# Performance work log

Hardware: AMD Instinct MI355X
Metric: run time of the kernel (lower is better)

The kernel has to match this reference:

```python
import jax, jax.numpy as jnp
import numpy as np

B, S, D, H = 2, 2048, 1024, 16
DH = D // H
EPS = 1e-5


def setup_inputs() -> dict:
    key = jax.random.key(0)
    ks = jax.random.split(key, 12)
    inp = {
        "Q_source": jax.random.normal(ks[0], (B, S, D), jnp.float32),
        "K_source": jax.random.normal(ks[1], (B, S, D), jnp.float32),
        "V_source": jax.random.normal(ks[2], (B, S, D), jnp.float32),
        "padding_mask": jnp.zeros((B, 1, 1, S), dtype=bool),  # no padded keys (avoids NaN rows)
        "future_mask": jnp.triu(jnp.ones((S, S), dtype=bool), k=1)[None, None],  # causal
    }
    sc = 1.0 / np.sqrt(D)
    names = ["WQ", "WK", "WV", "WO"]
    for i, n in enumerate(names):
        inp[n] = jax.random.normal(ks[3 + i], (D, D), jnp.float32) * sc
        inp["b" + n[1]] = jnp.zeros((D,), jnp.float32)
    inp["gamma"] = jnp.ones((D,), jnp.float32)
    inp["beta"] = jnp.zeros((D,), jnp.float32)
    return inp


def reference(Q_source, K_source, V_source, padding_mask, future_mask,
              WQ, bQ, WK, bK, WV, bV, WO, bO, gamma, beta):
    b = Q_source.shape[0]
    # torch Linear: x @ W.T + b ; reshape to [B, H, S, DH]
    def proj(x, W, bb):
        y = x @ W.T + bb
        return y.reshape(b, -1, H, DH).transpose(0, 2, 1, 3)

    Q = proj(Q_source, WQ, bQ)
    K = proj(K_source, WK, bK)
    V = proj(V_source, WV, bV)

    scores = jnp.einsum("bhqd,bhkd->bhqk", Q, K) / jnp.sqrt(jnp.float32(DH))
    neg_inf = jnp.float32(-jnp.inf)
    scores = jnp.where(padding_mask, neg_inf, scores)
    scores = jnp.where(future_mask, neg_inf, scores)
    attn = jax.nn.softmax(scores, axis=-1)

    ctx = jnp.einsum("bhqk,bhkd->bhqd", attn, V)
    ctx = ctx.transpose(0, 2, 1, 3).reshape(b, -1, D)
    out = ctx @ WO.T + bO

    x = Q_source + out
    mu = x.mean(-1, keepdims=True)
    var = x.var(-1, keepdims=True)
    return (x - mu) * jax.lax.rsqrt(var + EPS) * gamma + beta
```

## Files before the change

### kernel.cpp

```cpp
#include <hip/hip_runtime.h>

#define S_LEN 2048
#define DMODEL 1024
#define NH 16
#define DHD 64

typedef __attribute__((ext_vector_type(8))) short bh8;
typedef __attribute__((ext_vector_type(4))) float f32x4;
typedef __attribute__((ext_vector_type(2))) unsigned int u32x2;
typedef __attribute__((ext_vector_type(4))) unsigned int u32x4;
typedef unsigned short u16;
typedef unsigned int u32;

static __device__ __forceinline__ u16 f2bf(float f) {
    unsigned u = __builtin_bit_cast(unsigned, f);
    u += 0x7fffu + ((u >> 16) & 1u);
    return (u16)(u >> 16);
}

typedef const __attribute__((address_space(1))) void* gptr_t;
typedef __attribute__((address_space(3))) void* lptr_t;

static __device__ __forceinline__ void gll16(const void* g, void* l) {
    __builtin_amdgcn_global_load_lds((gptr_t)g, (lptr_t)l, 16, 0, 0);
}

__global__ __launch_bounds__(256) void cvt_all(const float* __restrict__ WQ, const float* __restrict__ WK,
                                               const float* __restrict__ WV, const float* __restrict__ WO,
                                               const float* __restrict__ S0, const float* __restrict__ S1,
                                               const float* __restrict__ S2,
                                               u16* __restrict__ wq, u16* __restrict__ wk,
                                               u16* __restrict__ wv, u16* __restrict__ wo,
                                               u16* __restrict__ q0, u16* __restrict__ k0,
                                               u16* __restrict__ v0) {
    int bid = blockIdx.x;
    const float* s;
    u16* o;
    size_t base;
    if (bid < 2048) {
        int wi = bid >> 9;
        s = wi == 0 ? WQ : (wi == 1 ? WK : (wi == 2 ? WV : WO));
        o = wi == 0 ? wq : (wi == 1 ? wk : (wi == 2 ? wv : wo));
        base = (size_t)(bid & 511) * 2048;
    } else {
        int r = bid - 2048;
        int si = r >> 11;
        s = si == 0 ? S0 : (si == 1 ? S1 : S2);
        o = si == 0 ? q0 : (si == 1 ? k0 : v0);
        base = (size_t)(r & 2047) * 2048;
    }
    size_t i = base + (size_t)threadIdx.x * 8;
    float4 a = *(const float4*)(s + i);
    float4 b = *(const float4*)(s + i + 4);
    u32 p0 = (u32)f2bf(a.x) | ((u32)f2bf(a.y) << 16);
    u32 p1 = (u32)f2bf(a.z) | ((u32)f2bf(a.w) << 16);
    u32 p2 = (u32)f2bf(b.x) | ((u32)f2bf(b.y) << 16);
    u32 p3 = (u32)f2bf(b.z) | ((u32)f2bf(b.w) << 16);
    *(u32x4*)(o + i) = (u32x4){p0, p1, p2, p3};
}

template <int BM, int OBF, int AF32>
static __device__ __forceinline__ void gemm_body(const void* __restrict__ Ap, const u16* __restrict__ Bm,
                                                 const float* __restrict__ bias, void* __restrict__ Cv,
                                                 int N, int K, int bi, int bj, short* Al, short* Bl,
                                                 float oscale) {
    constexpr int MI = BM / 32;
    constexpr int NC = BM / 64;
    int tid = threadIdx.x, lane = tid & 63, w = tid >> 6;
    int ln = lane & 15, hi = lane >> 4;
    int wm = w >> 1, wn = w & 1;
    f32x4 acc[MI][4];
#pragma unroll
    for (int i = 0; i < MI; i++)
#pragma unroll
        for (int j = 0; j < 4; j++) acc[i][j] = (f32x4){0.f, 0.f, 0.f, 0.f};
    int nk = K >> 5;

    float4 fa[NC][2];
    auto loadA = [&](int kt) {
#pragma unroll
        for (int c = 0; c < NC; ++c) {
            int o = c * 4096 + tid * 16;
            int row = o >> 6, e0 = (o & 63) >> 1;
            const float* src = (const float*)Ap + (size_t)(bi * BM + row) * K + kt * 32 + e0;
            fa[c][0] = *(const float4*)src;
            fa[c][1] = *(const float4*)(src + 4);
        }
    };
    auto writeA = [&](int buf) {
#pragma unroll
        for (int c = 0; c < NC; ++c) {
            int o = c * 4096 + tid * 16;
            u32 w0 = (u32)f2bf(fa[c][0].x) | ((u32)f2bf(fa[c][0].y) << 16);
            u32 w1 = (u32)f2bf(fa[c][0].z) | ((u32)f2bf(fa[c][0].w) << 16);
            u32 w2 = (u32)f2bf(fa[c][1].x) | ((u32)f2bf(fa[c][1].y) << 16);
            u32 w3 = (u32)f2bf(fa[c][1].z) | ((u32)f2bf(fa[c][1].w) << 16);
            *(u32x4*)((char*)(Al + buf * (BM * 32)) + o) = (u32x4){w0, w1, w2, w3};
        }
    };
    auto stageA_lds = [&](int buf, int kt) {
#pragma unroll
        for (int c = 0; c < NC; ++c) {
            int o = c * 4096 + tid * 16;
            int row = o >> 6, col = (o & 63) >> 1;
            gll16((const u16*)Ap + (size_t)(bi * BM + row) * K + kt * 32 + col,
                  (char*)(Al + buf * (BM * 32)) + o);
        }
    };
    auto stageB = [&](int buf, int kt) {
#pragma unroll
        for (int c = 0; c < 2; ++c) {
            int o = c * 4096 + tid * 16;
            int row = o >> 6, col = (o & 63) >> 1;
            gll16(Bm + (size_t)(bj * 128 + row) * K + kt * 32 + col, (char*)(Bl + buf * 4096) + o);
        }
    };

    if constexpr (AF32) { loadA(0); writeA(0); } else { stageA_lds(0, 0); }
    stageB(0, 0);
    __syncthreads();
    int cur = 0;
    for (int kt = 0; kt < nk; ++kt) {
        bool pre = (kt + 1 < nk);
        if (pre) {
            if constexpr (AF32) loadA(kt + 1); else stageA_lds(cur ^ 1, kt + 1);
            stageB(cur ^ 1, kt + 1);
        }
        bh8 av[MI], bv[4];
#pragma unroll
        for (int i = 0; i < MI; i++) av[i] = *(const bh8*)&Al[cur * (BM * 32) + (wm * (BM / 2) + i * 16 + ln) * 32 + hi * 8];
#pragma unroll
        for (int j = 0; j < 4; j++) bv[j] = *(const bh8*)&Bl[cur * 4096 + (wn * 64 + j * 16 + ln) * 32 + hi * 8];
#pragma unroll
        for (int i = 0; i < MI; i++)
#pragma unroll
            for (int j = 0; j < 4; j++)
                acc[i][j] = __builtin_amdgcn_mfma_f32_16x16x32_bf16(av[i], bv[j], acc[i][j], 0, 0, 0);
        if constexpr (AF32) { if (pre) writeA(cur ^ 1); }
        __syncthreads();
        cur ^= 1;
    }
    if constexpr (OBF == 2) {
#pragma unroll
        for (int j = 0; j < 4; j++) {
            int col = wn * 64 + j * 16 + ln;
            float bvs = bias[bj * 128 + col];
#pragma unroll
            for (int i = 0; i < MI; i++) {
                int row0 = wm * (BM / 2) + i * 16 + hi * 4;
                u32 p01 = (u32)f2bf(acc[i][j][0] + bvs) | ((u32)f2bf(acc[i][j][1] + bvs) << 16);
                u32 p23 = (u32)f2bf(acc[i][j][2] + bvs) | ((u32)f2bf(acc[i][j][3] + bvs) << 16);
                int idx = col * 128 + (row0 ^ ((col & 7) << 3));
                *(u32x2*)&Al[idx] = (u32x2){p01, p23};
            }
        }
        __syncthreads();
        int b = bi >> 4;
        int sbase = (bi & 15) * 128;
#pragma unroll
        for (int it = 0; it < 8; ++it) {
            int idx = it * 256 + tid;
            int dcol = idx >> 4;
            int sl = (idx & 15) * 8;
            bh8 v = *(const bh8*)&Al[dcol * 128 + (sl ^ ((dcol & 7) << 3))];
            int h = bj * 2 + (dcol >> 6), d = dcol & 63;
            *(bh8*)((u16*)Cv + ((size_t)((b * 16 + h) * 64 + d)) * 2048 + sbase + sl) = v;
        }
        return;
    }
#pragma unroll
    for (int j = 0; j < 4; j++) {
        int col = bj * 128 + wn * 64 + j * 16 + ln;
        float bvs = bias[col];
#pragma unroll
        for (int i = 0; i < MI; i++) {
            int row0 = bi * BM + wm * (BM / 2) + i * 16 + hi * 4;
#pragma unroll
            for (int rr = 0; rr < 4; rr++) {
                if (OBF) {
                    float v = (acc[i][j][rr] + bvs) * oscale;
                    ((u16*)Cv)[(size_t)(row0 + rr) * N + col] = f2bf(v);
                } else {
                    ((float*)Cv)[(size_t)(row0 + rr) * N + col] = acc[i][j][rr] + bvs;
                }
            }
        }
    }
}

__global__ __launch_bounds__(256, 3) void gemm_qkv(const u16* __restrict__ A0, const u16* __restrict__ A1,
                                                   const u16* __restrict__ A2, const u16* __restrict__ B0,
                                                   const u16* __restrict__ B1, const u16* __restrict__ B2,
                                                   const float* __restrict__ c0, const float* __restrict__ c1,
                                                   const float* __restrict__ c2, u16* __restrict__ C0,
                                                   u16* __restrict__ C1, u16* __restrict__ VT) {
    __shared__ short SH[16384];
    short* Al = SH;
    short* Bl = SH + 8192;
    int bid = blockIdx.x;
    int swz = (bid & 7) * 96 + (bid >> 3);
    int z = swz >> 8, t = swz & 255;
    if (z == 2) {
        gemm_body<128, 2, 0>(A2, B2, c2, VT, 1024, 1024, t >> 3, t & 7, Al, Bl, 1.0f);
    } else if (z == 0) {
        gemm_body<128, 1, 0>(A0, B0, c0, C0, 1024, 1024, t >> 3, t & 7, Al, Bl, 0.18033688f);
    } else {
        gemm_body<128, 1, 0>(A1, B1, c1, C1, 1024, 1024, t >> 3, t & 7, Al, Bl, 1.0f);
    }
}

__global__ __launch_bounds__(512, 4) void gemm_o(const u16* __restrict__ A, const u16* __restrict__ Bm,
                                                 const float* __restrict__ bias, float* __restrict__ C) {
    __shared__ short Al[2 * 64 * 32];
    __shared__ short Bl[2 * 128 * 32];
    int tid = threadIdx.x, lane = tid & 63, w = tid >> 6;
    int ln = lane & 15, hi = lane >> 4;
    int wm = w >> 2, wn = w & 3;
    int bid = blockIdx.x;
    int swz = (bid & 7) * 64 + (bid >> 3);
    int bi = swz >> 3, bj = swz & 7;
    f32x4 acc[2][2];
#pragma unroll
    for (int i = 0; i < 2; i++)
#pragma unroll
        for (int j = 0; j < 2; j++) acc[i][j] = (f32x4){0.f, 0.f, 0.f, 0.f};

    auto stageA = [&](int buf, int kt) {
        if (tid < 256) {
            int o = tid * 16;
            int row = o >> 6, col = (o & 63) >> 1;
            gll16(A + (size_t)(bi * 64 + row) * 1024 + kt * 32 + col, (char*)(Al + buf * 2048) + o);
        }
    };
    auto stageB = [&](int buf, int kt) {
        int o = tid * 16;
        int row = o >> 6, col = (o & 63) >> 1;
        gll16(Bm + (size_t)(bj * 128 + row) * 1024 + kt * 32 + col, (char*)(Bl + buf * 4096) + o);
    };

    stageA(0, 0);
    stageB(0, 0);
    __syncthreads();
    int cur = 0;
    for (int kt = 0; kt < 32; ++kt) {
        if (kt + 1 < 32) {
            stageA(cur ^ 1, kt + 1);
            stageB(cur ^ 1, kt + 1);
        }
        bh8 av[2], bv[2];
#pragma unroll
        for (int i = 0; i < 2; i++) av[i] = *(const bh8*)&Al[cur * 2048 + (wm * 32 + i * 16 + ln) * 32 + hi * 8];
#pragma unroll
        for (int j = 0; j < 2; j++) bv[j] = *(const bh8*)&Bl[cur * 4096 + (wn * 32 + j * 16 + ln) * 32 + hi * 8];
#pragma unroll
        for (int i = 0; i < 2; i++)
#pragma unroll
            for (int j = 0; j < 2; j++)
                acc[i][j] = __builtin_amdgcn_mfma_f32_16x16x32_bf16(av[i], bv[j], acc[i][j], 0, 0, 0);
        __syncthreads();
        cur ^= 1;
    }
#pragma unroll
    for (int j = 0; j < 2; j++) {
        int col = bj * 128 + wn * 32 + j * 16 + ln;
        float bvs = bias[col];
#pragma unroll
        for (int i = 0; i < 2; i++) {
            int row0 = bi * 64 + wm * 32 + i * 16 + hi * 4;
#pragma unroll
            for (int rr = 0; rr < 4; rr++)
                C[(size_t)(row0 + rr) * 1024 + col] = acc[i][j][rr] + bvs;
        }
    }
}

template <int PLO, int PHI>
static __device__ __forceinline__ void attn_core(const u16* __restrict__ Qp, const u16* __restrict__ Kp,
                                                 const u16* __restrict__ VT, u16* __restrict__ Ctx,
                                                 short* Klb, short* Vlb, short* Pw, float* Csh, float* Ls,
                                                 int b, int h, int bh, int qt, int tid) {
    int lane = tid & 63, w = tid >> 6;
    int grp = w >> 2;
    int qsub = w & 3;
    int tgl = tid & 255;
    int ln = lane & 15, hi = lane >> 4;
    __builtin_amdgcn_s_setprio(PLO);
    bh8 ones;
#pragma unroll
    for (int e = 0; e < 8; e++) ones[e] = (short)0x3F80;

    auto stage_kv = [&](int buf, int kt) {
#pragma unroll
        for (int c = 0; c < 2; ++c) {
            int o = c * 4096 + tgl * 16;
            int rr = o >> 7;
            int slot = (o >> 4) & 7;
            gll16(Kp + ((size_t)(b * S_LEN + kt * 64 + rr)) * DMODEL + h * DHD + ((slot ^ (rr & 7)) << 3),
                  (char*)(Klb + buf * 4096) + o);
            gll16(VT + ((size_t)(bh * DHD + rr)) * S_LEN + kt * 64 + ((slot ^ (rr & 7)) << 3),
                  (char*)(Vlb + buf * 4096) + o);
        }
    };

    int nh = qt + 1;
    int nt = 2 * qt + 2;
    int kbase = grp * nh;
    int qg0 = (qt << 7) + qsub * 32 + ln;
    const bh8* qr0 = (const bh8*)(Qp + ((size_t)(b * S_LEN + qg0)) * DMODEL + h * DHD);
    const bh8* qr1 = (const bh8*)(Qp + ((size_t)(b * S_LEN + qg0 + 16)) * DMODEL + h * DHD);
    bh8 qf[2][2];
    qf[0][0] = qr0[hi]; qf[0][1] = qr0[4 + hi];
    qf[1][0] = qr1[hi]; qf[1][1] = qr1[4 + hi];
    f32x4 ctxa[2][4];
    f32x4 lacc[2];
#pragma unroll
    for (int g = 0; g < 2; g++) {
        lacc[g] = (f32x4){0.f, 0.f, 0.f, 0.f};
#pragma unroll
        for (int i = 0; i < 4; i++) ctxa[g][i] = (f32x4){0.f, 0.f, 0.f, 0.f};
    }
    stage_kv(0, kbase);
    __syncthreads();
    int cur = 0;
    for (int i = 0; i < nh; ++i) {
        int kt = kbase + i;
        if (i + 1 < nh) stage_kv(cur ^ 1, kt + 1);
        f32x4 sc[2][4];
#pragma unroll
        for (int g = 0; g < 2; g++)
#pragma unroll
            for (int ks = 0; ks < 4; ++ks) sc[g][ks] = (f32x4){0.f, 0.f, 0.f, 0.f};
        __builtin_amdgcn_s_setprio(PHI);
#pragma unroll
        for (int dwin = 0; dwin < 2; ++dwin) {
#pragma unroll
            for (int ks = 0; ks < 4; ++ks) {
                int rr = ks * 16 + ln;
                bh8 kv = *(const bh8*)&Klb[cur * 4096 + rr * 64 + ((dwin * 32 + hi * 8) ^ ((rr & 7) << 3))];
                sc[0][ks] = __builtin_amdgcn_mfma_f32_16x16x32_bf16(kv, qf[0][dwin], sc[0][ks], 0, 0, 0);
                sc[1][ks] = __builtin_amdgcn_mfma_f32_16x16x32_bf16(kv, qf[1][dwin], sc[1][ks], 0, 0, 0);
            }
        }
        __builtin_amdgcn_s_setprio(PLO);
        if (kt >= nt - 2) {
#pragma unroll
            for (int g = 0; g < 2; g++) {
                int qgq = qg0 + g * 16;
#pragma unroll
                for (int ks = 0; ks < 4; ++ks)
#pragma unroll
                    for (int rr = 0; rr < 4; ++rr) {
                        int kg = kt * 64 + ks * 16 + hi * 4 + rr;
                        sc[g][ks][rr] = (kg <= qgq) ? sc[g][ks][rr] : -1e30f;
                    }
            }
        }
#pragma unroll
        for (int g = 0; g < 2; g++) {
#pragma unroll
            for (int ks = 0; ks < 4; ++ks) {
                u32 u0 = __builtin_bit_cast(u32, __builtin_amdgcn_exp2f(sc[g][ks][0]));
                u32 u1 = __builtin_bit_cast(u32, __builtin_amdgcn_exp2f(sc[g][ks][1]));
                u32 u2 = __builtin_bit_cast(u32, __builtin_amdgcn_exp2f(sc[g][ks][2]));
                u32 u3 = __builtin_bit_cast(u32, __builtin_amdgcn_exp2f(sc[g][ks][3]));
                u32 a01 = (u0 >> 16) | (u1 & 0xffff0000u);
                u32 a23 = (u2 >> 16) | (u3 & 0xffff0000u);
                int kloc = ks * 16 + hi * 4;
                *(u32x2*)&Pw[(g * 16 + ln) * 64 + (kloc ^ ((ln & 7) << 3))] = (u32x2){a01, a23};
            }
        }
        __builtin_amdgcn_s_setprio(PHI);
#pragma unroll
        for (int kw = 0; kw < 2; ++kw) {
            bh8 pf0 = *(const bh8*)&Pw[ln * 64 + ((kw * 32 + hi * 8) ^ ((ln & 7) << 3))];
            bh8 pf1 = *(const bh8*)&Pw[(16 + ln) * 64 + ((kw * 32 + hi * 8) ^ ((ln & 7) << 3))];
            lacc[0] = __builtin_amdgcn_mfma_f32_16x16x32_bf16(ones, pf0, lacc[0], 0, 0, 0);
            lacc[1] = __builtin_amdgcn_mfma_f32_16x16x32_bf16(ones, pf1, lacc[1], 0, 0, 0);
#pragma unroll
            for (int ds = 0; ds < 4; ++ds) {
                int d = ds * 16 + ln;
                bh8 vf = *(const bh8*)&Vlb[cur * 4096 + d * 64 + ((kw * 32 + hi * 8) ^ ((d & 7) << 3))];
                ctxa[0][ds] = __builtin_amdgcn_mfma_f32_16x16x32_bf16(vf, pf0, ctxa[0][ds], 0, 0, 0);
                ctxa[1][ds] = __builtin_amdgcn_mfma_f32_16x16x32_bf16(vf, pf1, ctxa[1][ds], 0, 0, 0);
            }
        }
        __builtin_amdgcn_s_setprio(PLO);
        __syncthreads();
        cur ^= 1;
    }
    __builtin_amdgcn_s_setprio(0);
    if (grp == 1) {
#pragma unroll
        for (int g = 0; g < 2; g++) {
            int qloc = g * 16 + ln;
#pragma unroll
            for (int ds = 0; ds < 4; ++ds) {
                int doff = (ds * 16 + hi * 4) ^ ((qloc & 7) << 3);
                *(f32x4*)&Csh[(qsub * 32 + qloc) * 64 + doff] = ctxa[g][ds];
            }
            if (hi == 0) Ls[qsub * 32 + qloc] = lacc[g][0];
        }
    }
    __syncthreads();
    if (grp == 0) {
#pragma unroll
        for (int g = 0; g < 2; g++) {
            int qloc = g * 16 + ln;
            float inv = 1.f / (lacc[g][0] + Ls[qsub * 32 + qloc]);
            u16* cp = Ctx + ((size_t)(b * S_LEN + qg0 + g * 16)) * DMODEL + h * DHD;
#pragma unroll
            for (int ds = 0; ds < 4; ++ds) {
                int doff = (ds * 16 + hi * 4) ^ ((qloc & 7) << 3);
                f32x4 p = *(const f32x4*)&Csh[(qsub * 32 + qloc) * 64 + doff];
                ushort4 st;
                st.x = f2bf((ctxa[g][ds][0] + p[0]) * inv);
                st.y = f2bf((ctxa[g][ds][1] + p[1]) * inv);
                st.z = f2bf((ctxa[g][ds][2] + p[2]) * inv);
                st.w = f2bf((ctxa[g][ds][3] + p[3]) * inv);
                *(ushort4*)(cp + ds * 16 + hi * 4) = st;
            }
        }
    }
}

__global__ __launch_bounds__(512, 1) void attn_fwd(const u16* __restrict__ Qp, const u16* __restrict__ Kp,
                                                   const u16* __restrict__ VT, u16* __restrict__ Ctx) {
    __shared__ short Kl[2][2][4096];
    __shared__ short Vl[2][2][4096];
    __shared__ short Pl[8][2048];
    __shared__ float Ls[128];
    int tid = threadIdx.x, w = tid >> 6;
    int grp = w >> 2;
    int bid = blockIdx.x;
    int rnd = bid >> 8, slot = bid & 255;
    int xcd = slot & 7, t = slot >> 3;
    int bh = xcd * 4 + (t & 3);
    int qte = t >> 2;
    int qt = rnd ? (15 - 2 * qte) : (2 * qte);
    int b = bh >> 4, h = bh & 15;
    float* Csh = (float*)&Kl[0][0][0];
    if (qt >= 8)
        attn_core<2, 3>(Qp, Kp, VT, Ctx, &Kl[grp][0][0], &Vl[grp][0][0], &Pl[w][0], Csh, Ls, b, h, bh, qt, tid);
    else
        attn_core<0, 1>(Qp, Kp, VT, Ctx, &Kl[grp][0][0], &Vl[grp][0][0], &Pl[w][0], Csh, Ls, b, h, bh, qt, tid);
}

__global__ __launch_bounds__(256) void ln_res(const float* __restrict__ Xres, const float* __restrict__ Y,
                                              const float* __restrict__ gamma, const float* __restrict__ beta,
                                              float* __restrict__ out) {
    int row = blockIdx.x, tid = threadIdx.x;
    const float4* xr = (const float4*)(Xres + (size_t)row * DMODEL);
    const float4* yr = (const float4*)(Y + (size_t)row * DMODEL);
    float4 a = xr[tid], bq = yr[tid];
    float x0 = a.x + bq.x, x1 = a.y + bq.y, x2 = a.z + bq.z, x3 = a.w + bq.w;
    float s1 = x0 + x1 + x2 + x3;
    float s2 = x0 * x0 + x1 * x1 + x2 * x2 + x3 * x3;
#pragma unroll
    for (int off = 32; off > 0; off >>= 1) {
        s1 += __shfl_xor(s1, off);
        s2 += __shfl_xor(s2, off);
    }
    __shared__ float r1[4], r2[4];
    int wv = tid >> 6;
    if ((tid & 63) == 0) { r1[wv] = s1; r2[wv] = s2; }
    __syncthreads();
    s1 = r1[0] + r1[1] + r1[2] + r1[3];
    s2 = r2[0] + r2[1] + r2[2] + r2[3];
    float mu = s1 * (1.0f / 1024.0f);
    float var = s2 * (1.0f / 1024.0f) - mu * mu;
    float rstd = rsqrtf(var + 1e-5f);
    const float4* g4 = (const float4*)gamma;
    const float4* b4 = (const float4*)beta;
    float4 g = g4[tid], bb = b4[tid];
    float4 res;
    res.x = (x0 - mu) * rstd * g.x + bb.x;
    res.y = (x1 - mu) * rstd * g.y + bb.y;
    res.z = (x2 - mu) * rstd * g.z + bb.z;
    res.w = (x3 - mu) * rstd * g.w + bb.w;
    *((float4*)(out + (size_t)row * DMODEL) + tid) = res;
}

extern "C" void kernel_launch(void* const* d_in, const int* in_sizes, int n_in,
                              void* d_out, int out_size, void* d_ws, size_t ws_size,
                              hipStream_t stream) {
    const float* Qs = (const float*)d_in[0];
    const float* Ks = (const float*)d_in[1];
    const float* Vs = (const float*)d_in[2];
    const float* WQ = (const float*)d_in[5];
    const float* bQ = (const float*)d_in[6];
    const float* WK = (const float*)d_in[7];
    const float* bK = (const float*)d_in[8];
    const float* WV = (const float*)d_in[9];
    const float* bV = (const float*)d_in[10];
    const float* WO = (const float*)d_in[11];
    const float* bO = (const float*)d_in[12];
    const float* gamma = (const float*)d_in[13];
    const float* beta = (const float*)d_in[14];

    const size_t MB = 1u << 20;
    char* w8 = (char*)d_ws;
    u16* Qb  = (u16*)(w8 + 0 * MB);
    u16* Kb  = (u16*)(w8 + 8 * MB);
    u16* Vb  = (u16*)(w8 + 16 * MB);
    u16* WQb = (u16*)(w8 + 24 * MB);
    u16* WKb = (u16*)(w8 + 26 * MB);
    u16* WVb = (u16*)(w8 + 28 * MB);
    u16* WOb = (u16*)(w8 + 30 * MB);
    u16* Qp  = (u16*)(w8 + 32 * MB);
    u16* Kp  = (u16*)(w8 + 40 * MB);
    u16* VTb = (u16*)(w8 + 56 * MB);
    u16* Ctx = (u16*)(w8 + 64 * MB);
    float* Y2 = (float*)(w8 + 72 * MB);

    cvt_all<<<8192, 256, 0, stream>>>(WQ, WK, WV, WO, Qs, Ks, Vs, WQb, WKb, WVb, WOb, Qb, Kb, Vb);
    gemm_qkv<<<768, 256, 0, stream>>>(Qb, Kb, Vb, WQb, WKb, WVb, bQ, bK, bV, Qp, Kp, VTb);
    attn_fwd<<<512, 512, 0, stream>>>(Qp, Kp, VTb, Ctx);
    gemm_o<<<512, 512, 0, stream>>>(Ctx, WOb, bO, Y2);
    ln_res<<<4096, 256, 0, stream>>>(Qs, Y2, gamma, beta, (float*)d_out);
}
```

Measured before the change: 112.3 us.

## Process two KV tiles per attention iteration and fuse residual add into output GEMM

The attention inner loop now handles two 64-key tiles per iteration with a four-deep K/V shared-memory ring. This halves the number of block-wide barriers and gives more independent MFMA work between syncs. Shared-memory use doubles for K/V, and the Ls scratch now aliases part of the P buffer. Separately, the residual add moves into the output-projection GEMM epilogue, so the layernorm kernel reads one input array instead of two.

After: 109.8 us. 1.02x faster.

```diff
diff --git a/kernel.cpp b/kernel.cpp
--- a/kernel.cpp
+++ b/kernel.cpp
@@ -210,7 +210,8 @@
 }
 
 __global__ __launch_bounds__(512, 4) void gemm_o(const u16* __restrict__ A, const u16* __restrict__ Bm,
-                                                 const float* __restrict__ bias, float* __restrict__ C) {
+                                                 const float* __restrict__ bias, const float* __restrict__ Res,
+                                                 float* __restrict__ C) {
     __shared__ short Al[2 * 64 * 32];
     __shared__ short Bl[2 * 128 * 32];
     int tid = threadIdx.x, lane = tid & 63, w = tid >> 6;
@@ -268,8 +269,10 @@
         for (int i = 0; i < 2; i++) {
             int row0 = bi * 64 + wm * 32 + i * 16 + hi * 4;
 #pragma unroll
-            for (int rr = 0; rr < 4; rr++)
-                C[(size_t)(row0 + rr) * 1024 + col] = acc[i][j][rr] + bvs;
+            for (int rr = 0; rr < 4; rr++) {
+                size_t idx = (size_t)(row0 + rr) * 1024 + col;
+                C[idx] = acc[i][j][rr] + bvs + Res[idx];
+            }
         }
     }
 }
@@ -320,29 +323,47 @@
         for (int i = 0; i < 4; i++) ctxa[g][i] = (f32x4){0.f, 0.f, 0.f, 0.f};
     }
     stage_kv(0, kbase);
+    if (nh > 1) stage_kv(1, kbase + 1);
     __syncthreads();
-    int cur = 0;
-    for (int i = 0; i < nh; ++i) {
-        int kt = kbase + i;
-        if (i + 1 < nh) stage_kv(cur ^ 1, kt + 1);
-        f32x4 sc[2][4];
+    for (int i = 0; i < nh; i += 2) {
+        int s = i >> 1;
+        int b0 = (s & 1) << 1;
+        int b1 = b0 + 1;
+        bool two = (i + 1 < nh);
+        if (i + 2 < nh) stage_kv(b0 ^ 2, kbase + i + 2);
+        if (i + 3 < nh) stage_kv(b1 ^ 2, kbase + i + 3);
+        int kt0 = kbase + i;
+        int kt1 = kbase + i + 1;
+        f32x4 scA[2][4], scB[2][4];
 #pragma unroll
         for (int g = 0; g < 2; g++)
 #pragma unroll
-            for (int ks = 0; ks < 4; ++ks) sc[g][ks] = (f32x4){0.f, 0.f, 0.f, 0.f};
+            for (int ks = 0; ks < 4; ++ks) { scA[g][ks] = (f32x4){0.f, 0.f, 0.f, 0.f}; scB[g][ks] = (f32x4){0.f, 0.f, 0.f, 0.f}; }
         __builtin_amdgcn_s_setprio(PHI);
 #pragma unroll
         for (int dwin = 0; dwin < 2; ++dwin) {
 #pragma unroll
             for (int ks = 0; ks < 4; ++ks) {
                 int rr = ks * 16 + ln;
-                bh8 kv = *(const bh8*)&Klb[cur * 4096 + rr * 64 + ((dwin * 32 + hi * 8) ^ ((rr & 7) << 3))];
-                sc[0][ks] = __builtin_amdgcn_mfma_f32_16x16x32_bf16(kv, qf[0][dwin], sc[0][ks], 0, 0, 0);
-                sc[1][ks] = __builtin_amdgcn_mfma_f32_16x16x32_bf16(kv, qf[1][dwin], sc[1][ks], 0, 0, 0);
+                bh8 kv = *(const bh8*)&Klb[b0 * 4096 + rr * 64 + ((dwin * 32 + hi * 8) ^ ((rr & 7) << 3))];
+                scA[0][ks] = __builtin_amdgcn_mfma_f32_16x16x32_bf16(kv, qf[0][dwin], scA[0][ks], 0, 0, 0);
+                scA[1][ks] = __builtin_amdgcn_mfma_f32_16x16x32_bf16(kv, qf[1][dwin], scA[1][ks], 0, 0, 0);
+            }
+        }
+        if (two) {
+#pragma unroll
+            for (int dwin = 0; dwin < 2; ++dwin) {
+#pragma unroll
+                for (int ks = 0; ks < 4; ++ks) {
+                    int rr = ks * 16 + ln;
+                    bh8 kv = *(const bh8*)&Klb[b1 * 4096 + rr * 64 + ((dwin * 32 + hi * 8) ^ ((rr & 7) << 3))];
+                    scB[0][ks] = __builtin_amdgcn_mfma_f32_16x16x32_bf16(kv, qf[0][dwin], scB[0][ks], 0, 0, 0);
+                    scB[1][ks] = __builtin_amdgcn_mfma_f32_16x16x32_bf16(kv, qf[1][dwin], scB[1][ks], 0, 0, 0);
+                }
             }
         }
         __builtin_amdgcn_s_setprio(PLO);
-        if (kt >= nt - 2) {
+        if (kt0 >= nt - 2) {
 #pragma unroll
             for (int g = 0; g < 2; g++) {
                 int qgq = qg0 + g * 16;
@@ -350,8 +371,8 @@
                 for (int ks = 0; ks < 4; ++ks)
 #pragma unroll
                     for (int rr = 0; rr < 4; ++rr) {
-                        int kg = kt * 64 + ks * 16 + hi * 4 + rr;
-                        sc[g][ks][rr] = (kg <= qgq) ? sc[g][ks][rr] : -1e30f;
+                        int kg = kt0 * 64 + ks * 16 + hi * 4 + rr;
+                        scA[g][ks][rr] = (kg <= qgq) ? scA[g][ks][rr] : -1e30f;
                     }
             }
         }
@@ -359,10 +380,10 @@
         for (int g = 0; g < 2; g++) {
 #pragma unroll
             for (int ks = 0; ks < 4; ++ks) {
-                u32 u0 = __builtin_bit_cast(u32, __builtin_amdgcn_exp2f(sc[g][ks][0]));
-                u32 u1 = __builtin_bit_cast(u32, __builtin_amdgcn_exp2f(sc[g][ks][1]));
-                u32 u2 = __builtin_bit_cast(u32, __builtin_amdgcn_exp2f(sc[g][ks][2]));
-                u32 u3 = __builtin_bit_cast(u32, __builtin_amdgcn_exp2f(sc[g][ks][3]));
+                u32 u0 = __builtin_bit_cast(u32, __builtin_amdgcn_exp2f(scA[g][ks][0]));
+                u32 u1 = __builtin_bit_cast(u32, __builtin_amdgcn_exp2f(scA[g][ks][1]));
+                u32 u2 = __builtin_bit_cast(u32, __builtin_amdgcn_exp2f(scA[g][ks][2]));
+                u32 u3 = __builtin_bit_cast(u32, __builtin_amdgcn_exp2f(scA[g][ks][3]));
                 u32 a01 = (u0 >> 16) | (u1 & 0xffff0000u);
                 u32 a23 = (u2 >> 16) | (u3 & 0xffff0000u);
                 int kloc = ks * 16 + hi * 4;
@@ -379,14 +400,58 @@
 #pragma unroll
             for (int ds = 0; ds < 4; ++ds) {
                 int d = ds * 16 + ln;
-                bh8 vf = *(const bh8*)&Vlb[cur * 4096 + d * 64 + ((kw * 32 + hi * 8) ^ ((d & 7) << 3))];
+                bh8 vf = *(const bh8*)&Vlb[b0 * 4096 + d * 64 + ((kw * 32 + hi * 8) ^ ((d & 7) << 3))];
                 ctxa[0][ds] = __builtin_amdgcn_mfma_f32_16x16x32_bf16(vf, pf0, ctxa[0][ds], 0, 0, 0);
                 ctxa[1][ds] = __builtin_amdgcn_mfma_f32_16x16x32_bf16(vf, pf1, ctxa[1][ds], 0, 0, 0);
             }
         }
         __builtin_amdgcn_s_setprio(PLO);
+        if (two) {
+            if (kt1 >= nt - 2) {
+#pragma unroll
+                for (int g = 0; g < 2; g++) {
+                    int qgq = qg0 + g * 16;
+#pragma unroll
+                    for (int ks = 0; ks < 4; ++ks)
+#pragma unroll
+                        for (int rr = 0; rr < 4; ++rr) {
+                            int kg = kt1 * 64 + ks * 16 + hi * 4 + rr;
+                            scB[g][ks][rr] = (kg <= qgq) ? scB[g][ks][rr] : -1e30f;
+                        }
+                }
+            }
+#pragma unroll
+            for (int g = 0; g < 2; g++) {
+#pragma unroll
+                for (int ks = 0; ks < 4; ++ks) {
+                    u32 u0 = __builtin_bit_cast(u32, __builtin_amdgcn_exp2f(scB[g][ks][0]));
+                    u32 u1 = __builtin_bit_cast(u32, __builtin_amdgcn_exp2f(scB[g][ks][1]));
+                    u32 u2 = __builtin_bit_cast(u32, __builtin_amdgcn_exp2f(scB[g][ks][2]));
+                    u32 u3 = __builtin_bit_cast(u32, __builtin_amdgcn_exp2f(scB[g][ks][3]));
+                    u32 a01 = (u0 >> 16) | (u1 & 0xffff0000u);
+                    u32 a23 = (u2 >> 16) | (u3 & 0xffff0000u);
+                    int kloc = ks * 16 + hi * 4;
+                    *(u32x2*)&Pw[(g * 16 + ln) * 64 + (kloc ^ ((ln & 7) << 3))] = (u32x2){a01, a23};
+                }
+            }
+            __builtin_amdgcn_s_setprio(PHI);
+#pragma unroll
+            for (int kw = 0; kw < 2; ++kw) {
+                bh8 pf0 = *(const bh8*)&Pw[ln * 64 + ((kw * 32 + hi * 8) ^ ((ln & 7) << 3))];
+                bh8 pf1 = *(const bh8*)&Pw[(16 + ln) * 64 + ((kw * 32 + hi * 8) ^ ((ln & 7) << 3))];
+                lacc[0] = __builtin_amdgcn_mfma_f32_16x16x32_bf16(ones, pf0, lacc[0], 0, 0, 0);
+                lacc[1] = __builtin_amdgcn_mfma_f32_16x16x32_bf16(ones, pf1, lacc[1], 0, 0, 0);
+#pragma unroll
+                for (int ds = 0; ds < 4; ++ds) {
+                    int d = ds * 16 + ln;
+                    bh8 vf = *(const bh8*)&Vlb[b1 * 4096 + d * 64 + ((kw * 32 + hi * 8) ^ ((d & 7) << 3))];
+                    ctxa[0][ds] = __builtin_amdgcn_mfma_f32_16x16x32_bf16(vf, pf0, ctxa[0][ds], 0, 0, 0);
+                    ctxa[1][ds] = __builtin_amdgcn_mfma_f32_16x16x32_bf16(vf, pf1, ctxa[1][ds], 0, 0, 0);
+                }
+            }
+            __builtin_amdgcn_s_setprio(PLO);
+        }
         __syncthreads();
-        cur ^= 1;
     }
     __builtin_amdgcn_s_setprio(0);
     if (grp == 1) {
@@ -425,10 +490,9 @@
 
 __global__ __launch_bounds__(512, 1) void attn_fwd(const u16* __restrict__ Qp, const u16* __restrict__ Kp,
                                                    const u16* __restrict__ VT, u16* __restrict__ Ctx) {
-    __shared__ short Kl[2][2][4096];
-    __shared__ short Vl[2][2][4096];
+    __shared__ short Kl[2][4][4096];
+    __shared__ short Vl[2][4][4096];
     __shared__ short Pl[8][2048];
-    __shared__ float Ls[128];
     int tid = threadIdx.x, w = tid >> 6;
     int grp = w >> 2;
     int bid = blockIdx.x;
@@ -439,20 +503,20 @@
     int qt = rnd ? (15 - 2 * qte) : (2 * qte);
     int b = bh >> 4, h = bh & 15;
     float* Csh = (float*)&Kl[0][0][0];
+    float* Ls = (float*)&Pl[7][1024];
     if (qt >= 8)
         attn_core<2, 3>(Qp, Kp, VT, Ctx, &Kl[grp][0][0], &Vl[grp][0][0], &Pl[w][0], Csh, Ls, b, h, bh, qt, tid);
     else
         attn_core<0, 1>(Qp, Kp, VT, Ctx, &Kl[grp][0][0], &Vl[grp][0][0], &Pl[w][0], Csh, Ls, b, h, bh, qt, tid);
 }
 
-__global__ __launch_bounds__(256) void ln_res(const float* __restrict__ Xres, const float* __restrict__ Y,
+__global__ __launch_bounds__(256) void ln_res(const float* __restrict__ Y,
                                               const float* __restrict__ gamma, const float* __restrict__ beta,
                                               float* __restrict__ out) {
     int row = blockIdx.x, tid = threadIdx.x;
-    const float4* xr = (const float4*)(Xres + (size_t)row * DMODEL);
     const float4* yr = (const float4*)(Y + (size_t)row * DMODEL);
-    float4 a = xr[tid], bq = yr[tid];
-    float x0 = a.x + bq.x, x1 = a.y + bq.y, x2 = a.z + bq.z, x3 = a.w + bq.w;
+    float4 a = yr[tid];
+    float x0 = a.x, x1 = a.y, x2 = a.z, x3 = a.w;
     float s1 = x0 + x1 + x2 + x3;
     float s2 = x0 * x0 + x1 * x1 + x2 * x2 + x3 * x3;
 #pragma unroll
@@ -515,6 +579,6 @@
     cvt_all<<<8192, 256, 0, stream>>>(WQ, WK, WV, WO, Qs, Ks, Vs, WQb, WKb, WVb, WOb, Qb, Kb, Vb);
     gemm_qkv<<<768, 256, 0, stream>>>(Qb, Kb, Vb, WQb, WKb, WVb, bQ, bK, bV, Qp, Kp, VTb);
     attn_fwd<<<512, 512, 0, stream>>>(Qp, Kp, VTb, Ctx);
-    gemm_o<<<512, 512, 0, stream>>>(Ctx, WOb, bO, Y2);
-    ln_res<<<4096, 256, 0, stream>>>(Qs, Y2, gamma, beta, (float*)d_out);
-}
+    gemm_o<<<512, 512, 0, stream>>>(Ctx, WOb, bO, Qs, Y2);
+    ln_res<<<4096, 256, 0, stream>>>(Y2, gamma, beta, (float*)d_out);
+}
```
